# Performance work log

Hardware: AMD Instinct MI355X
Metric: run time of the kernel (lower is better)

## Reference

```python
import jax, jax.numpy as jnp
import numpy as np

B, T, D, H = 2, 2048, 2048, 16
HD = D // H
SCALE = HD ** -0.5
NEG_INF = float('-inf')


def setup_inputs() -> dict:
    key = jax.random.key(0)
    ks = jax.random.split(key, 10)
    x = jax.random.normal(ks[0], (B, T, D), dtype=jnp.float32)
    # causal float mask: 0 on/below diagonal, -inf above (broadcast over B, H)
    causal = jnp.triu(jnp.ones((T, T), dtype=bool), k=1)
    mask = jnp.where(causal, NEG_INF, 0.0).astype(jnp.float32)[None, None]
    # xavier_uniform for [D, D]: bound = sqrt(6 / (D + D))
    bound = float(np.sqrt(6.0 / (D + D)))
    def xav(k):
        return jax.random.uniform(k, (D, D), jnp.float32, -bound, bound)
    wq, wk, wv, wo = xav(ks[1]), xav(ks[2]), xav(ks[3]), xav(ks[4])
    # biases: uniform_[0,1)
    bq = jax.random.uniform(ks[5], (D,), jnp.float32)
    bk = jax.random.uniform(ks[6], (D,), jnp.float32)
    bv = jax.random.uniform(ks[7], (D,), jnp.float32)
    bo = jax.random.uniform(ks[8], (D,), jnp.float32)
    return {"x": x, "mask": mask, "wq": wq, "bq": bq, "wk": wk, "bk": bk,
            "wv": wv, "bv": bv, "wo": wo, "bo": bo}


def reference(x, mask, wq, bq, wk, bk, wv, bv, wo, bo):
    b, t, d = x.shape
    def split_heads(y):  # [B,T,D] -> [B,H,T,HD]
        return y.reshape(b, t, H, HD).transpose(0, 2, 1, 3)
    q = split_heads(x @ wq.T + bq)
    k = split_heads(x @ wk.T + bk)
    v = split_heads(x @ wv.T + bv)
    scores = jnp.einsum('bhqd,bhkd->bhqk', q, k) * SCALE
    scores = jnp.where(mask == NEG_INF, NEG_INF, scores)
    attn = jax.nn.softmax(scores, axis=-1)
    out = jnp.einsum('bhqk,bhkd->bhqd', attn, v)  # [B,H,T,HD]
    out = out.transpose(0, 2, 1, 3).reshape(b, t, d)
    return out @ wo.T + bo
```

## Files before the change

### kernel.cpp

```cpp
#include <hip/hip_runtime.h>

typedef unsigned short u16;
typedef __bf16 bf16x8 __attribute__((ext_vector_type(8)));
typedef float f32x4 __attribute__((ext_vector_type(4)));

constexpr int B_ = 2, T_ = 2048, D_ = 2048, H_ = 16, HD_ = 128;
constexpr int MROWS = B_ * T_;
constexpr int KD = D_;
constexpr int ND = D_;
#define SL2E (0.08838834764831845f * 1.4426950408889634f)

__device__ __forceinline__ u16 f2bf(float f) {
  unsigned u = __float_as_uint(f);
  u += 0x7FFF + ((u >> 16) & 1);
  return (u16)(u >> 16);
}

__device__ __forceinline__ float fexp2(float x) { return __builtin_amdgcn_exp2f(x); }

__device__ __forceinline__ void async16(const void* g, void* l) {
  __builtin_amdgcn_global_load_lds((__attribute__((address_space(1))) void*)g,
                                   (__attribute__((address_space(3))) void*)l,
                                   16, 0, 0);
}

__global__ void cvt_kernel(const float* __restrict__ in, u16* __restrict__ out, int n) {
  int i = (blockIdx.x * blockDim.x + threadIdx.x) * 4;
  if (i >= n) return;
  const float4 v = *(const float4*)(in + i);
  ushort4 h;
  h.x = f2bf(v.x); h.y = f2bf(v.y); h.z = f2bf(v.z); h.w = f2bf(v.w);
  *(ushort4*)(out + i) = h;
}

__global__ void cvt4_kernel(const float* __restrict__ w0, const float* __restrict__ w1,
                            const float* __restrict__ w2, const float* __restrict__ w3,
                            u16* __restrict__ o0, u16* __restrict__ o1,
                            u16* __restrict__ o2, u16* __restrict__ o3, int n) {
  const float* in = blockIdx.y == 0 ? w0 : blockIdx.y == 1 ? w1 : blockIdx.y == 2 ? w2 : w3;
  u16* out = blockIdx.y == 0 ? o0 : blockIdx.y == 1 ? o1 : blockIdx.y == 2 ? o2 : o3;
  int i = (blockIdx.x * blockDim.x + threadIdx.x) * 4;
  if (i >= n) return;
  const float4 v = *(const float4*)(in + i);
  ushort4 h;
  h.x = f2bf(v.x); h.y = f2bf(v.y); h.z = f2bf(v.z); h.w = f2bf(v.w);
  *(ushort4*)(out + i) = h;
}

template <int MODE>
__device__ __forceinline__ void gemm_body(const u16* __restrict__ A,
                                          const u16* __restrict__ Bw,
                                          const float* __restrict__ bias,
                                          void* __restrict__ outp,
                                          u16* As, u16* Bs) {
  constexpr int BK = 32;
  const int tid = threadIdx.x;
  const int wave = tid >> 6;
  const int lane = tid & 63;
  const int quad = lane >> 4;
  const int l16 = lane & 15;
  const int wm = (wave >> 1) * 64;
  const int wn = (wave & 1) * 64;
  const int mBase = blockIdx.y * 128;
  const int nBase = blockIdx.x * 128;

  f32x4 acc[4][4] = {};

  const int srow = wave * 32 + (lane >> 2);
  const int soff = ((lane & 3) ^ ((lane >> 3) & 3)) * 8;
  const u16* Ag = A + (size_t)(mBase + srow) * KD + soff;
  const u16* Bg = Bw + (size_t)(nBase + srow) * KD + soff;
  u16* AsW0 = &As[(wave * 32) * BK];
  u16* AsW1 = &As[(wave * 32 + 16) * BK];
  u16* BsW0 = &Bs[(wave * 32) * BK];
  u16* BsW1 = &Bs[(wave * 32 + 16) * BK];

  const int sw = (quad ^ ((l16 >> 1) & 3)) * 8;

  for (int k0 = 0; k0 < KD; k0 += BK) {
    __syncthreads();
    async16(Ag + k0, AsW0);
    async16(Ag + 16 * KD + k0, AsW1);
    async16(Bg + k0, BsW0);
    async16(Bg + 16 * KD + k0, BsW1);
    __syncthreads();

    bf16x8 a[4], b[4];
#pragma unroll
    for (int i = 0; i < 4; i++)
      a[i] = *(const bf16x8*)&As[(wm + i * 16 + l16) * BK + sw];
#pragma unroll
    for (int j = 0; j < 4; j++)
      b[j] = *(const bf16x8*)&Bs[(wn + j * 16 + l16) * BK + sw];
#pragma unroll
    for (int i = 0; i < 4; i++)
#pragma unroll
      for (int j = 0; j < 4; j++)
        acc[i][j] = __builtin_amdgcn_mfma_f32_16x16x32_bf16(a[i], b[j], acc[i][j], 0, 0, 0);
  }

  float* outF = (float*)outp;
  u16* outH = (u16*)outp;
#pragma unroll
  for (int i = 0; i < 4; i++) {
#pragma unroll
    for (int j = 0; j < 4; j++) {
      const int col = nBase + wn + j * 16 + l16;
      const float bv = bias[col];
#pragma unroll
      for (int r = 0; r < 4; r++) {
        const int row = mBase + wm + i * 16 + quad * 4 + r;
        const float v = acc[i][j][r] + bv;
        if (MODE == 0) {
          outH[(size_t)row * ND + col] = f2bf(v);
        } else if (MODE == 1) {
          const int bb = row >> 11;
          const int t = row & (T_ - 1);
          const int h = col >> 7;
          const int d = col & (HD_ - 1);
          outH[(size_t)(((bb * H_ + h) << 7) + d) * T_ + t] = f2bf(v);
        } else {
          outF[(size_t)row * ND + col] = v;
        }
      }
    }
  }
}

__global__ __launch_bounds__(256) void gemm_qkv(const u16* __restrict__ A,
                                                const u16* __restrict__ Wq, const u16* __restrict__ Wk,
                                                const u16* __restrict__ Wv,
                                                const float* __restrict__ bq, const float* __restrict__ bk,
                                                const float* __restrict__ bv,
                                                u16* __restrict__ Qo, u16* __restrict__ Ko,
                                                u16* __restrict__ Vo) {
  __shared__ u16 As[128 * 32];
  __shared__ u16 Bs[128 * 32];
  const int z = blockIdx.z;
  const u16* Bw = z == 0 ? Wq : z == 1 ? Wk : Wv;
  const float* bias = z == 0 ? bq : z == 1 ? bk : bv;
  if (z == 2)
    gemm_body<1>(A, Bw, bias, (void*)Vo, As, Bs);
  else
    gemm_body<0>(A, Bw, bias, (void*)(z == 0 ? Qo : Ko), As, Bs);
}

__global__ __launch_bounds__(256) void gemm_out(const u16* __restrict__ A, const u16* __restrict__ Bw,
                                                const float* __restrict__ bias, float* __restrict__ outp) {
  __shared__ u16 As[128 * 32];
  __shared__ u16 Bs[128 * 32];
  gemm_body<2>(A, Bw, bias, (void*)outp, As, Bs);
}

constexpr int PSTR = 72;

__global__ __launch_bounds__(256, 2) void attn_kernel(const u16* __restrict__ Q,
                                                      const u16* __restrict__ Kc,
                                                      const u16* __restrict__ Vt,
                                                      u16* __restrict__ O) {
  __shared__ u16 Ks[2][64 * 128];
  __shared__ u16 Vs[2][128 * 64];
  __shared__ u16 Ps[4 * 16 * PSTR];
  const int tid = threadIdx.x;
  const int wave = tid >> 6;
  const int lane = tid & 63;
  const int quad = lane >> 4;
  const int l16 = lane & 15;
  const int lo = blockIdx.x;
  const int hi = 31 - lo;
  const int bh = blockIdx.y;
  const int b = bh >> 4;
  const int h = bh & 15;

  const int tIdx[2] = {lo, hi};

  bf16x8 qf[2][4];
#pragma unroll
  for (int t = 0; t < 2; t++) {
    const u16* Qp = Q + (size_t)(b * T_ + tIdx[t] * 64 + wave * 16 + l16) * D_ + h * HD_;
#pragma unroll
    for (int kc = 0; kc < 4; kc++)
      qf[t][kc] = *(const bf16x8*)(Qp + kc * 32 + quad * 8);
  }

  f32x4 o[2][8] = {};
  float mrow[2], lrow[2];
#pragma unroll
  for (int t = 0; t < 2; t++) { mrow[t] = -__builtin_huge_valf(); lrow[t] = 0.f; }

  const u16* Kg = Kc + (size_t)(b * T_) * D_ + h * HD_;
  const u16* Vg = Vt + (size_t)((b * H_ + h) * HD_) * T_;
  u16* Pw = &Ps[wave * 16 * PSTR];
  const int swz = (l16 & 7);

  const u16* kgp[4];
  int klo[4];
  const u16* vgp[4];
  int vlo[4];
#pragma unroll
  for (int c = 0; c < 4; c++) {
    const int krl = wave * 16 + c * 4 + (lane >> 4);
    const int kch = (lane & 15) ^ (krl & 7);
    kgp[c] = Kg + (size_t)krl * D_ + kch * 8;
    klo[c] = (wave * 16 + c * 4) * 128;
    const int vrl = wave * 32 + c * 8 + (lane >> 3);
    const int vch = (lane & 7) ^ (vrl & 7);
    vgp[c] = Vg + (size_t)vrl * T_ + vch * 8;
    vlo[c] = (wave * 32 + c * 8) * 64;
  }

#pragma unroll
  for (int c = 0; c < 4; c++) async16(kgp[c], &Ks[0][klo[c]]);
#pragma unroll
  for (int c = 0; c < 4; c++) async16(vgp[c], &Vs[0][vlo[c]]);

  for (int kt = 0; kt <= hi; kt++) {
    const int cur = kt & 1;
    __syncthreads();

    if (kt < hi) {
      const int nxt = cur ^ 1;
#pragma unroll
      for (int c = 0; c < 4; c++) async16(kgp[c] + (size_t)(kt + 1) * 64 * D_, &Ks[nxt][klo[c]]);
#pragma unroll
      for (int c = 0; c < 4; c++) async16(vgp[c] + (size_t)(kt + 1) * 64, &Vs[nxt][vlo[c]]);
    }

#pragma unroll
    for (int t = 0; t < 2; t++) {
      if (t == 0 && kt > lo) continue;

      f32x4 st[4];
#pragma unroll
      for (int nt = 0; nt < 4; nt++) {
        f32x4 a = {};
#pragma unroll
        for (int kc = 0; kc < 4; kc++) {
          const int pos = (kc * 4 + quad) ^ swz;
          bf16x8 kf = *(const bf16x8*)&Ks[cur][(nt * 16 + l16) * 128 + pos * 8];
          a = __builtin_amdgcn_mfma_f32_16x16x32_bf16(kf, qf[t][kc], a, 0, 0, 0);
        }
        st[nt] = a;
      }

      const bool diag = (kt == tIdx[t]);
#pragma unroll
      for (int nt = 0; nt < 4; nt++)
#pragma unroll
        for (int r = 0; r < 4; r++) {
          float v = st[nt][r] * SL2E;
          if (diag) {
            const int kcol = nt * 16 + quad * 4 + r;
            const int qrow = wave * 16 + l16;
            if (kcol > qrow) v = -__builtin_huge_valf();
          }
          st[nt][r] = v;
        }

      float mx = st[0][0];
#pragma unroll
      for (int nt = 0; nt < 4; nt++)
#pragma unroll
        for (int r = 0; r < 4; r++) mx = fmaxf(mx, st[nt][r]);
      mx = fmaxf(mx, __shfl_xor(mx, 16));
      mx = fmaxf(mx, __shfl_xor(mx, 32));
      const float mnew = fmaxf(mrow[t], mx);
      const float alpha = fexp2(mrow[t] - mnew);
      mrow[t] = mnew;
      float sum = 0.f;
#pragma unroll
      for (int nt = 0; nt < 4; nt++)
#pragma unroll
        for (int r = 0; r < 4; r++) {
          const float p = fexp2(st[nt][r] - mnew);
          st[nt][r] = p;
          sum += p;
        }
      sum += __shfl_xor(sum, 16);
      sum += __shfl_xor(sum, 32);
      lrow[t] = lrow[t] * alpha + sum;

      float af[4];
#pragma unroll
      for (int r = 0; r < 4; r++) af[r] = __shfl(alpha, quad * 4 + r);
#pragma unroll
      for (int dt = 0; dt < 8; dt++)
#pragma unroll
        for (int r = 0; r < 4; r++)
          o[t][dt][r] *= af[r];

#pragma unroll
      for (int nt = 0; nt < 4; nt++) {
        ushort4 pk;
        pk.x = f2bf(st[nt][0]); pk.y = f2bf(st[nt][1]);
        pk.z = f2bf(st[nt][2]); pk.w = f2bf(st[nt][3]);
        *(ushort4*)&Pw[l16 * PSTR + nt * 16 + quad * 4] = pk;
      }

      bf16x8 pf[2];
#pragma unroll
      for (int kc = 0; kc < 2; kc++)
        pf[kc] = *(const bf16x8*)&Pw[l16 * PSTR + kc * 32 + quad * 8];
#pragma unroll
      for (int dt = 0; dt < 8; dt++) {
#pragma unroll
        for (int kc = 0; kc < 2; kc++) {
          const int pos = (kc * 4 + quad) ^ swz;
          bf16x8 vf = *(const bf16x8*)&Vs[cur][(dt * 16 + l16) * 64 + pos * 8];
          o[t][dt] = __builtin_amdgcn_mfma_f32_16x16x32_bf16(pf[kc], vf, o[t][dt], 0, 0, 0);
        }
      }
    }
  }

#pragma unroll
  for (int t = 0; t < 2; t++) {
    float linv[4];
#pragma unroll
    for (int r = 0; r < 4; r++) linv[r] = 1.f / __shfl(lrow[t], quad * 4 + r);
#pragma unroll
    for (int dt = 0; dt < 8; dt++)
#pragma unroll
      for (int r = 0; r < 4; r++) {
        const int rowg = b * T_ + tIdx[t] * 64 + wave * 16 + quad * 4 + r;
        const int col = h * HD_ + dt * 16 + l16;
        O[(size_t)rowg * D_ + col] = f2bf(o[t][dt][r] * linv[r]);
      }
  }
}

extern "C" void kernel_launch(void* const* d_in, const int* in_sizes, int n_in,
                              void* d_out, int out_size, void* d_ws, size_t ws_size,
                              hipStream_t stream) {
  (void)in_sizes; (void)n_in; (void)out_size; (void)ws_size;
  const float* x  = (const float*)d_in[0];
  const float* wq = (const float*)d_in[2];
  const float* bq = (const float*)d_in[3];
  const float* wk = (const float*)d_in[4];
  const float* bk = (const float*)d_in[5];
  const float* wv = (const float*)d_in[6];
  const float* bv = (const float*)d_in[7];
  const float* wo = (const float*)d_in[8];
  const float* bo = (const float*)d_in[9];

  u16* ws  = (u16*)d_ws;
  u16* xb  = ws;
  u16* wqb = ws + 8388608;
  u16* wkb = ws + 12582912;
  u16* wvb = ws + 16777216;
  u16* wob = ws + 20971520;
  u16* Qb  = ws + 25165824;
  u16* Kb  = ws + 33554432;
  u16* Vtb = ws + 41943040;
  u16* Ob  = ws + 50331648;

  cvt_kernel<<<8192, 256, 0, stream>>>(x, xb, 8388608);
  cvt4_kernel<<<dim3(4096, 4), 256, 0, stream>>>(wq, wk, wv, wo, wqb, wkb, wvb, wob, 4194304);

  dim3 gg(ND / 128, MROWS / 128, 3);
  gemm_qkv<<<gg, 256, 0, stream>>>(xb, wqb, wkb, wvb, bq, bk, bv, Qb, Kb, Vtb);
  attn_kernel<<<dim3(16, B_ * H_), 256, 0, stream>>>(Qb, Kb, Vtb, Ob);
  gemm_out<<<dim3(ND / 128, MROWS / 128), 256, 0, stream>>>(Ob, wob, bo, (float*)d_out);
}
```

Measured before the change: 396.5 us.

## Replace QKV GEMM with 256x256-tile 8-wave pipelined kernel

Replaces the 128x128-tile QKV projection GEMM with a 512-thread kernel that computes 256x256 tiles with a 64-wide K step. It double-buffers LDS through async global-to-LDS loads, uses XOR-swizzled LDS addressing, and interleaves MFMA quadrants with barriers and s_setprio. Blocks are remapped across XCDs for L2 locality. The aim is more data reuse per loaded byte and overlap of loads with compute, at the cost of higher register and LDS pressure (128KB LDS per block) and fragile hand-written waitcnt/barrier scheduling.

```diff
diff --git a/kernel.cpp b/kernel.cpp
--- a/kernel.cpp
+++ b/kernel.cpp
@@ -23,6 +23,8 @@
                                    (__attribute__((address_space(3))) void*)l,
                                    16, 0, 0);
 }
+
+#define MEMFENCE asm volatile("" ::: "memory")
 
 __global__ void cvt_kernel(const float* __restrict__ in, u16* __restrict__ out, int n) {
   int i = (blockIdx.x * blockDim.x + threadIdx.x) * 4;
@@ -127,29 +129,195 @@
   }
 }
 
-__global__ __launch_bounds__(256) void gemm_qkv(const u16* __restrict__ A,
-                                                const u16* __restrict__ Wq, const u16* __restrict__ Wk,
-                                                const u16* __restrict__ Wv,
-                                                const float* __restrict__ bq, const float* __restrict__ bk,
-                                                const float* __restrict__ bv,
-                                                u16* __restrict__ Qo, u16* __restrict__ Ko,
-                                                u16* __restrict__ Vo) {
-  __shared__ u16 As[128 * 32];
-  __shared__ u16 Bs[128 * 32];
-  const int z = blockIdx.z;
-  const u16* Bw = z == 0 ? Wq : z == 1 ? Wk : Wv;
-  const float* bias = z == 0 ? bq : z == 1 ? bk : bv;
-  if (z == 2)
-    gemm_body<1>(A, Bw, bias, (void*)Vo, As, Bs);
-  else
-    gemm_body<0>(A, Bw, bias, (void*)(z == 0 ? Qo : Ko), As, Bs);
-}
-
 __global__ __launch_bounds__(256) void gemm_out(const u16* __restrict__ A, const u16* __restrict__ Bw,
                                                 const float* __restrict__ bias, float* __restrict__ outp) {
   __shared__ u16 As[128 * 32];
   __shared__ u16 Bs[128 * 32];
   gemm_body<2>(A, Bw, bias, (void*)outp, As, Bs);
+}
+
+constexpr int NT8 = KD / 64;
+constexpr int TILE8 = 256 * 64;
+
+__global__ __launch_bounds__(512, 2) void gemm_qkv8(
+    const u16* __restrict__ A,
+    const u16* __restrict__ Wq, const u16* __restrict__ Wk, const u16* __restrict__ Wv,
+    const float* __restrict__ bq, const float* __restrict__ bk, const float* __restrict__ bv,
+    u16* __restrict__ Qo, u16* __restrict__ Ko, u16* __restrict__ Vo) {
+  __shared__ u16 As[2 * TILE8];
+  __shared__ u16 Bs[2 * TILE8];
+
+  const int tid = threadIdx.x;
+  const int wave = tid >> 6;
+  const int lane = tid & 63;
+  const int quad = lane >> 4;
+  const int l16 = lane & 15;
+  const int wm = wave >> 2;
+  const int wn = wave & 3;
+
+  const int orig = blockIdx.x;
+  const int wg = (orig & 7) * 48 + (orig >> 3);
+  const int bx = wg % 24;
+  const int by = wg / 24;
+  const int mBase = by * 256;
+  const int nGlob = bx * 256;
+  const int z = nGlob >> 11;
+  const int nB = nGlob & (D_ - 1);
+  const u16* Bw = z == 0 ? Wq : z == 1 ? Wk : Wv;
+  const float* bias = z == 0 ? bq : z == 1 ? bk : bv;
+
+  const int lr = lane >> 3;
+  const int lcE = ((lane & 7) ^ lr) * 8;
+  const u16* Ag = A + (size_t)mBase * KD + lcE;
+  const u16* Bg = Bw + (size_t)nB * KD + lcE;
+  int sRow[4], sLds[4];
+#pragma unroll
+  for (int h = 0; h < 2; h++)
+#pragma unroll
+    for (int c = 0; c < 2; c++) {
+      const int rl = h * 128 + (c * 8 + wave) * 8;
+      sRow[h * 2 + c] = rl + lr;
+      sLds[h * 2 + c] = rl * 64;
+    }
+
+  const int csw0 = (quad ^ (l16 & 7)) * 8;
+  const int csw1 = ((4 + quad) ^ (l16 & 7)) * 8;
+
+  f32x4 acc[8][4] = {};
+  bf16x8 a[4][2], b0[2][2], b1[2][2];
+
+#pragma unroll
+  for (int t = 0; t < 2; t++) {
+    u16* AsD = As + t * TILE8;
+    u16* BsD = Bs + t * TILE8;
+#pragma unroll
+    for (int k = 0; k < 4; k++) async16(Bg + (size_t)sRow[k] * KD + t * 64, BsD + sLds[k]);
+#pragma unroll
+    for (int k = 0; k < 4; k++) async16(Ag + (size_t)sRow[k] * KD + t * 64, AsD + sLds[k]);
+  }
+  asm volatile("s_waitcnt vmcnt(8)" ::: "memory");
+  __builtin_amdgcn_s_barrier();
+  MEMFENCE;
+
+#pragma unroll 2
+  for (int t = 0; t < NT8; ++t) {
+    const int cur = t & 1;
+    const u16* AsC = As + cur * TILE8;
+    const u16* BsC = Bs + cur * TILE8;
+    u16* AsS = (u16*)AsC;
+    u16* BsS = (u16*)BsC;
+
+#pragma unroll
+    for (int i = 0; i < 4; i++) {
+      const int r = (wm * 128 + i * 16 + l16) * 64;
+      a[i][0] = *(const bf16x8*)&AsC[r + csw0];
+      a[i][1] = *(const bf16x8*)&AsC[r + csw1];
+    }
+#pragma unroll
+    for (int j = 0; j < 2; j++) {
+      const int r = (wn * 64 + j * 16 + l16) * 64;
+      b0[j][0] = *(const bf16x8*)&BsC[r + csw0];
+      b0[j][1] = *(const bf16x8*)&BsC[r + csw1];
+    }
+    MEMFENCE; __builtin_amdgcn_s_barrier(); MEMFENCE;
+    __builtin_amdgcn_s_setprio(1);
+#pragma unroll
+    for (int i = 0; i < 4; i++)
+#pragma unroll
+      for (int j = 0; j < 2; j++) {
+        acc[i][j] = __builtin_amdgcn_mfma_f32_16x16x32_bf16(a[i][0], b0[j][0], acc[i][j], 0, 0, 0);
+        acc[i][j] = __builtin_amdgcn_mfma_f32_16x16x32_bf16(a[i][1], b0[j][1], acc[i][j], 0, 0, 0);
+      }
+    __builtin_amdgcn_s_setprio(0);
+    MEMFENCE; __builtin_amdgcn_s_barrier(); MEMFENCE;
+
+#pragma unroll
+    for (int j = 0; j < 2; j++) {
+      const int r = (wn * 64 + 32 + j * 16 + l16) * 64;
+      b1[j][0] = *(const bf16x8*)&BsC[r + csw0];
+      b1[j][1] = *(const bf16x8*)&BsC[r + csw1];
+    }
+    MEMFENCE; __builtin_amdgcn_s_barrier(); MEMFENCE;
+    __builtin_amdgcn_s_setprio(1);
+#pragma unroll
+    for (int i = 0; i < 4; i++)
+#pragma unroll
+      for (int j = 0; j < 2; j++) {
+        acc[i][2 + j] = __builtin_amdgcn_mfma_f32_16x16x32_bf16(a[i][0], b1[j][0], acc[i][2 + j], 0, 0, 0);
+        acc[i][2 + j] = __builtin_amdgcn_mfma_f32_16x16x32_bf16(a[i][1], b1[j][1], acc[i][2 + j], 0, 0, 0);
+      }
+    __builtin_amdgcn_s_setprio(0);
+    MEMFENCE; __builtin_amdgcn_s_barrier(); MEMFENCE;
+
+#pragma unroll
+    for (int i = 0; i < 4; i++) {
+      const int r = (wm * 128 + 64 + i * 16 + l16) * 64;
+      a[i][0] = *(const bf16x8*)&AsC[r + csw0];
+      a[i][1] = *(const bf16x8*)&AsC[r + csw1];
+    }
+    if (t + 2 < NT8) {
+#pragma unroll
+      for (int k = 0; k < 4; k++)
+        async16(Bg + (size_t)sRow[k] * KD + (t + 2) * 64, BsS + sLds[k]);
+    }
+    MEMFENCE; __builtin_amdgcn_s_barrier(); MEMFENCE;
+    __builtin_amdgcn_s_setprio(1);
+#pragma unroll
+    for (int i = 0; i < 4; i++)
+#pragma unroll
+      for (int j = 0; j < 2; j++) {
+        acc[4 + i][2 + j] = __builtin_amdgcn_mfma_f32_16x16x32_bf16(a[i][0], b1[j][0], acc[4 + i][2 + j], 0, 0, 0);
+        acc[4 + i][2 + j] = __builtin_amdgcn_mfma_f32_16x16x32_bf16(a[i][1], b1[j][1], acc[4 + i][2 + j], 0, 0, 0);
+      }
+    __builtin_amdgcn_s_setprio(0);
+    MEMFENCE; __builtin_amdgcn_s_barrier(); MEMFENCE;
+
+    if (t + 2 < NT8) {
+#pragma unroll
+      for (int k = 0; k < 4; k++)
+        async16(Ag + (size_t)sRow[k] * KD + (t + 2) * 64, AsS + sLds[k]);
+    }
+    MEMFENCE; __builtin_amdgcn_s_barrier(); MEMFENCE;
+    __builtin_amdgcn_s_setprio(1);
+#pragma unroll
+    for (int i = 0; i < 4; i++)
+#pragma unroll
+      for (int j = 0; j < 2; j++) {
+        acc[4 + i][j] = __builtin_amdgcn_mfma_f32_16x16x32_bf16(a[i][0], b0[j][0], acc[4 + i][j], 0, 0, 0);
+        acc[4 + i][j] = __builtin_amdgcn_mfma_f32_16x16x32_bf16(a[i][1], b0[j][1], acc[4 + i][j], 0, 0, 0);
+      }
+    __builtin_amdgcn_s_setprio(0);
+    if (t + 2 < NT8) {
+      asm volatile("s_waitcnt vmcnt(8)" ::: "memory");
+    } else {
+      asm volatile("s_waitcnt vmcnt(0)" ::: "memory");
+    }
+    MEMFENCE; __builtin_amdgcn_s_barrier(); MEMFENCE;
+  }
+
+  u16* outH = z == 0 ? Qo : Ko;
+#pragma unroll
+  for (int j = 0; j < 4; j++) {
+    const int col = nB + wn * 64 + j * 16 + l16;
+    const float bvv = bias[col];
+#pragma unroll
+    for (int i = 0; i < 8; i++) {
+#pragma unroll
+      for (int r = 0; r < 4; r++) {
+        const int row = mBase + wm * 128 + i * 16 + quad * 4 + r;
+        const float v = acc[i][j][r] + bvv;
+        if (z == 2) {
+          const int bb = row >> 11;
+          const int tt = row & (T_ - 1);
+          const int hh = col >> 7;
+          const int dd = col & (HD_ - 1);
+          Vo[(size_t)(((bb * H_ + hh) << 7) + dd) * T_ + tt] = f2bf(v);
+        } else {
+          outH[(size_t)row * ND + col] = f2bf(v);
+        }
+      }
+    }
+  }
 }
 
 constexpr int PSTR = 72;
@@ -357,8 +525,7 @@
   cvt_kernel<<<8192, 256, 0, stream>>>(x, xb, 8388608);
   cvt4_kernel<<<dim3(4096, 4), 256, 0, stream>>>(wq, wk, wv, wo, wqb, wkb, wvb, wob, 4194304);
 
-  dim3 gg(ND / 128, MROWS / 128, 3);
-  gemm_qkv<<<gg, 256, 0, stream>>>(xb, wqb, wkb, wvb, bq, bk, bv, Qb, Kb, Vtb);
+  gemm_qkv8<<<384, 512, 0, stream>>>(xb, wqb, wkb, wvb, bq, bk, bv, Qb, Kb, Vtb);
   attn_kernel<<<dim3(16, B_ * H_), 256, 0, stream>>>(Qb, Kb, Vtb, Ob);
   gemm_out<<<dim3(ND / 128, MROWS / 128), 256, 0, stream>>>(Ob, wob, bo, (float*)d_out);
 }
```

Measured after the change: 429.0 us. 8.2% more time.
